# Optimization experiments

Measured on AMD Instinct MI355X. Metric: run time of the kernel, lower is better.

Reference implementation:

```python
import jax, jax.numpy as jnp
import numpy as np

DIM = 1024
HEADS = 16
HEAD_DIM = DIM // HEADS
LAYERS = 8
HIDDEN = 4 * DIM
VOCAB = 266
MAX_POS = 32768
B = 4
L = 2048
SCALE = HEAD_DIM ** -0.5
EPS = 1e-5


def layer_norm(x, g, b):
    m = jnp.mean(x, axis=-1, keepdims=True)
    v = jnp.mean(jnp.square(x - m), axis=-1, keepdims=True)
    return (x - m) * jax.lax.rsqrt(v + EPS) * g + b


def setup_inputs() -> dict:
    key = jax.random.key(0)
    ks = jax.random.split(key, 16)
    s = 0.02
    return {
        "tokens": jax.random.randint(ks[0], (B, L), 0, VOCAB),
        "tok_emb": jax.random.normal(ks[1], (VOCAB, DIM), jnp.float32) * s,
        "pos_emb": jax.random.normal(ks[2], (MAX_POS, DIM), jnp.float32) * s,
        "ln1_g": jnp.ones((LAYERS, DIM), jnp.float32),
        "ln1_b": jnp.zeros((LAYERS, DIM), jnp.float32),
        "q_w": jax.random.normal(ks[3], (LAYERS, DIM, DIM), jnp.float32) * s,
        "k_w": jax.random.normal(ks[4], (LAYERS, DIM, DIM), jnp.float32) * s,
        "v_w": jax.random.normal(ks[5], (LAYERS, DIM, DIM), jnp.float32) * s,
        "o_w": jax.random.normal(ks[6], (LAYERS, DIM, DIM), jnp.float32) * s,
        "ln2_g": jnp.ones((LAYERS, DIM), jnp.float32),
        "ln2_b": jnp.zeros((LAYERS, DIM), jnp.float32),
        "w1_w": jax.random.normal(ks[7], (LAYERS, HIDDEN, DIM), jnp.float32) * s,
        "wg_w": jax.random.normal(ks[8], (LAYERS, HIDDEN, DIM), jnp.float32) * s,
        "w2_w": jax.random.normal(ks[9], (LAYERS, DIM, HIDDEN), jnp.float32) * s,
        "lnf_g": jnp.ones((DIM,), jnp.float32),
        "lnf_b": jnp.zeros((DIM,), jnp.float32),
        "lm_w": jax.random.normal(ks[10], (VOCAB, DIM), jnp.float32) * s,
    }


def reference(tokens, tok_emb, pos_emb, ln1_g, ln1_b, q_w, k_w, v_w, o_w,
              ln2_g, ln2_b, w1_w, wg_w, w2_w, lnf_g, lnf_b, lm_w):
    Bv, Lv = tokens.shape
    x = tok_emb[tokens] + pos_emb[jnp.arange(Lv)][None, :, :]  # [B,L,D]
    # strictly-upper-triangular causal mask (True = masked)
    rows = jnp.arange(Lv)
    mask = rows[None, :] > rows[:, None]  # [L,L], col > row
    pos_bias = jnp.arange(Lv, dtype=x.dtype) * 0.01  # [L]
    neg_inf = jnp.array(-jnp.inf, dtype=x.dtype)

    for i in range(LAYERS):
        h = layer_norm(x, ln1_g[i], ln1_b[i])
        q = jnp.einsum('bld,ed->ble', h, q_w[i]).reshape(Bv, Lv, HEADS, HEAD_DIM).transpose(0, 2, 1, 3)
        k = jnp.einsum('bld,ed->ble', h, k_w[i]).reshape(Bv, Lv, HEADS, HEAD_DIM).transpose(0, 2, 1, 3)
        v = jnp.einsum('bld,ed->ble', h, v_w[i]).reshape(Bv, Lv, HEADS, HEAD_DIM).transpose(0, 2, 1, 3)
        attn = jnp.einsum('bhqd,bhkd->bhqk', q, k) * SCALE
        attn = jnp.where(mask[None, None, :, :], neg_inf, attn)
        attn = attn + pos_bias[None, None, None, :]
        attn = jax.nn.softmax(attn, axis=-1)
        out = jnp.einsum('bhqk,bhkd->bhqd', attn, v).transpose(0, 2, 1, 3).reshape(Bv, Lv, DIM)
        attn_out = jnp.einsum('bld,ed->ble', out, o_w[i])
        x = x + attn_out
        h2 = layer_norm(x, ln2_g[i], ln2_b[i])
        ff = jnp.einsum('blh,dh->bld', jax.nn.silu(jnp.einsum('bld,hd->blh', h2, w1_w[i])) * jnp.einsum('bld,hd->blh', h2, wg_w[i]), w2_w[i])
        x = x + ff

    last = layer_norm(x[:, -1, :], lnf_g, lnf_b)  # [B, D]
    return jnp.einsum('bd,vd->bv', last, lm_w)  # [B, VOCAB]
```

## Files before the change

### kernel.cpp

```cpp
#include <hip/hip_runtime.h>
#include <hip/hip_bf16.h>
#include <math.h>

#define DIMD 1024
#define HEADS 16
#define HD 64
#define LAYERS 8
#define HIDDEN 4096
#define VOCAB 266
#define NB 4
#define SEQ 2048
#define ROWS (NB*SEQ)
#define LOG2E 1.4426950408889634f
#define QSCALE (0.125f * LOG2E)
#define BIAS2 (0.01f * LOG2E)
#define THR2 8.0f

typedef float f32x4 __attribute__((ext_vector_type(4)));
typedef float f32x16 __attribute__((ext_vector_type(16)));
typedef __bf16 bf16x8 __attribute__((ext_vector_type(8)));
typedef __bf16 bf16x4 __attribute__((ext_vector_type(4)));

__device__ __forceinline__ f32x4 mfma16(bf16x8 a, bf16x8 b, f32x4 c) {
    return __builtin_amdgcn_mfma_f32_16x16x32_bf16(a, b, c, 0, 0, 0);
}
__device__ __forceinline__ f32x16 mfma32(bf16x8 a, bf16x8 b, f32x16 c) {
    return __builtin_amdgcn_mfma_f32_32x32x16_bf16(a, b, c, 0, 0, 0);
}

__device__ __forceinline__ void gload16(const __bf16* g, __bf16* l) {
    __builtin_amdgcn_global_load_lds(
        (const __attribute__((address_space(1))) void*)g,
        (__attribute__((address_space(3))) void*)l, 16, 0, 0);
}

__device__ __forceinline__ unsigned pack2(float a, float b) {
    union { __bf16 h[2]; unsigned u; } t;
    t.h[0] = (__bf16)a; t.h[1] = (__bf16)b;
    return t.u;
}
union PUN8 { unsigned u[4]; bf16x8 v; };

__global__ void embed_kernel(const int* __restrict__ tok, const float* __restrict__ te,
                             const float* __restrict__ pe, float* __restrict__ x) {
    int row = blockIdx.x;
    int t = tok[row];
    int l = row & (SEQ - 1);
    int c = threadIdx.x;
    f32x4 tv = *(const f32x4*)(te + (size_t)t * DIMD + c * 4);
    f32x4 pv = *(const f32x4*)(pe + (size_t)l * DIMD + c * 4);
    *(f32x4*)(x + (size_t)row * DIMD + c * 4) = tv + pv;
}

__global__ void cvt_kernel(const float* q, const float* k, const float* v, const float* o,
                           const float* w1, const float* wg, const float* w2,
                           __bf16* __restrict__ dst) {
    const size_t MM = 1024 * 1024;
    const float* src; size_t n; size_t off; int ilv = 0;
    switch (blockIdx.y) {
        case 0: src = q;  n = MM;     off = 0;       break;
        case 1: src = k;  n = MM;     off = MM;      break;
        case 2: src = v;  n = MM;     off = 2 * MM;  break;
        case 3: src = o;  n = MM;     off = 3 * MM;  break;
        case 4: src = w1; n = 4 * MM; off = 4 * MM;  ilv = 1; break;
        case 5: src = wg; n = 4 * MM; off = 4 * MM;  ilv = 2; break;
        default: src = w2; n = 4 * MM; off = 12 * MM; break;
    }
    size_t stride = (size_t)gridDim.x * blockDim.x * 8;
    for (size_t i = ((size_t)blockIdx.x * blockDim.x + threadIdx.x) * 8; i < n; i += stride) {
        f32x4 a = *(const f32x4*)(src + i);
        f32x4 b = *(const f32x4*)(src + i + 4);
        bf16x8 ov;
        ov[0] = (__bf16)a[0]; ov[1] = (__bf16)a[1]; ov[2] = (__bf16)a[2]; ov[3] = (__bf16)a[3];
        ov[4] = (__bf16)b[0]; ov[5] = (__bf16)b[1]; ov[6] = (__bf16)b[2]; ov[7] = (__bf16)b[3];
        size_t di;
        if (ilv) {
            size_t row = i >> 10, col = i & 1023;
            di = off + (((row << 1) | (ilv - 1)) << 10) + col;
        } else {
            di = off + i;
        }
        *(bf16x8*)(dst + di) = ov;
    }
}

template<bool F32OUT>
__global__ void ln_kernel(const float* __restrict__ xin, size_t row_stride,
                          const float* __restrict__ g, const float* __restrict__ bb,
                          void* __restrict__ out) {
    int row = blockIdx.x;
    int c = threadIdx.x;
    const float* xr = xin + (size_t)row * row_stride;
    f32x4 v = *(const f32x4*)(xr + c * 4);
    float s = v[0] + v[1] + v[2] + v[3];
    float s2 = v[0]*v[0] + v[1]*v[1] + v[2]*v[2] + v[3]*v[3];
    #pragma unroll
    for (int o = 32; o; o >>= 1) { s += __shfl_xor(s, o); s2 += __shfl_xor(s2, o); }
    __shared__ float red[8];
    int w = c >> 6, lane = c & 63;
    if (lane == 0) { red[w] = s; red[4 + w] = s2; }
    __syncthreads();
    s = red[0] + red[1] + red[2] + red[3];
    s2 = red[4] + red[5] + red[6] + red[7];
    float mean = s * (1.f / DIMD);
    float var = s2 * (1.f / DIMD) - mean * mean;
    float rstd = rsqrtf(var + 1e-5f);
    f32x4 gv = *(const f32x4*)(g + c * 4);
    f32x4 bv = *(const f32x4*)(bb + c * 4);
    f32x4 o4;
    #pragma unroll
    for (int j = 0; j < 4; ++j) o4[j] = (v[j] - mean) * rstd * gv[j] + bv[j];
    if (F32OUT) {
        *(f32x4*)((float*)out + (size_t)row * DIMD + c * 4) = o4;
    } else {
        bf16x4 hv;
        #pragma unroll
        for (int j = 0; j < 4; ++j) hv[j] = (__bf16)o4[j];
        *(bf16x4*)((__bf16*)out + (size_t)row * DIMD + c * 4) = hv;
    }
}

template<int EPI>
__global__ __launch_bounds__(256, 4)
void gemm_bt(const __bf16* __restrict__ A, const __bf16* __restrict__ W,
             int M, int N, int K,
             __bf16* bdst, float* fdst, float scale) {
    __shared__ __bf16 As[128 * 64];
    __shared__ __bf16 Bs[128 * 64];
    int tid = threadIdx.x;
    int lane = tid & 63, w = tid >> 6;
    int wm = w >> 1, wn = w & 1;
    int g16 = lane >> 4, l16 = lane & 15;
    int m0 = blockIdx.y * 128, n0 = blockIdx.x * 128;
    f32x4 acc[4][4] = {};
    int trow = tid >> 3;
    int cs8 = ((tid & 7) ^ (trow & 7)) * 8;
    const __bf16* ga = A + (size_t)(m0 + trow) * K + cs8;
    const __bf16* gb = W + (size_t)(n0 + trow) * K + cs8;
    int xsw = (l16 & 7) << 4;

    for (int k0 = 0; k0 < K; k0 += 64) {
        #pragma unroll
        for (int p = 0; p < 4; ++p) {
            gload16(ga + (size_t)(p * 32) * K + k0, As + (p * 256 + w * 64) * 8);
            gload16(gb + (size_t)(p * 32) * K + k0, Bs + (p * 256 + w * 64) * 8);
        }
        __syncthreads();
        #pragma unroll
        for (int kk = 0; kk < 2; ++kk) {
            bf16x8 af[4], bfv[4];
            #pragma unroll
            for (int f = 0; f < 4; ++f) {
                int ar = wm * 64 + f * 16 + l16;
                int br = wn * 64 + f * 16 + l16;
                af[f]  = *(const bf16x8*)((const char*)As + ((ar * 128 + kk * 64 + g16 * 16) ^ xsw));
                bfv[f] = *(const bf16x8*)((const char*)Bs + ((br * 128 + kk * 64 + g16 * 16) ^ xsw));
            }
            #pragma unroll
            for (int fm = 0; fm < 4; ++fm)
                #pragma unroll
                for (int fn = 0; fn < 4; ++fn)
                    acc[fm][fn] = mfma16(af[fm], bfv[fn], acc[fm][fn]);
        }
        __syncthreads();
    }

    #pragma unroll
    for (int fm = 0; fm < 4; ++fm) {
        int rbase = m0 + wm * 64 + fm * 16 + g16 * 4;
        #pragma unroll
        for (int fn = 0; fn < 4; ++fn) {
            int col = n0 + wn * 64 + fn * 16 + l16;
            if (EPI == 2) {
                #pragma unroll
                for (int j = 0; j < 4; ++j) {
                    size_t idx = (size_t)(rbase + j) * N + col;
                    fdst[idx] += acc[fm][fn][j];
                }
            } else if (EPI == 5) {
                int which = col >> 10;
                int c = col & 1023;
                int hh = c >> 6, d = c & 63;
                if (which == 2) {
                    int b = rbase >> 11, l = rbase & 2047;
                    __bf16* vp = bdst + 2 * (size_t)ROWS * DIMD;
                    bf16x4 hv;
                    #pragma unroll
                    for (int j = 0; j < 4; ++j) hv[j] = (__bf16)acc[fm][fn][j];
                    *(bf16x4*)(vp + ((size_t)(b * HEADS + hh) * HD + d) * SEQ + l) = hv;
                } else {
                    float sc = (which == 0) ? scale : 1.f;
                    __bf16* base = bdst + (size_t)which * ROWS * DIMD;
                    #pragma unroll
                    for (int j = 0; j < 4; ++j) {
                        int row = rbase + j;
                        int b = row >> 11, l = row & 2047;
                        base[(((size_t)(b * HEADS + hh) * SEQ + l) << 6) + d] =
                            (__bf16)(acc[fm][fn][j] * sc);
                    }
                }
            } else if (EPI == 6) {
                #pragma unroll
                for (int j = 0; j < 4; ++j) {
                    float own = acc[fm][fn][j];
                    float other = __shfl_xor(own, 1);
                    if (!(l16 & 1)) {
                        float si = own / (1.f + __expf(-own));
                        bdst[(size_t)(rbase + j) * (N >> 1) + (col >> 1)] = (__bf16)(si * other);
                    }
                }
            }
        }
    }
}

__global__ __launch_bounds__(256, 2)
void attn_kernel(const __bf16* __restrict__ qt, const __bf16* __restrict__ kt,
                 const __bf16* __restrict__ vt, __bf16* __restrict__ ao) {
    int qtile = 15 - (blockIdx.x >> 6);
    int g = blockIdx.x & 63;
    int hh = g & 15, b = g >> 4;
    int tid = threadIdx.x, lane = tid & 63, w = tid >> 6;
    int l32 = lane & 31, hi = lane >> 5;

    __shared__ __bf16 Ks[2][64 * 64];
    __shared__ __bf16 Vs[2][64 * 64];

    const __bf16* qbase = qt + (size_t)(b * HEADS + hh) * SEQ * HD;
    const __bf16* kbase = kt + (size_t)(b * HEADS + hh) * SEQ * HD;
    const __bf16* vbase = vt + (size_t)(b * HEADS + hh) * HD * SEQ;

    int rr = lane >> 3;
    int cs8 = ((lane & 7) ^ rr) * 8;

    int qb = qtile * 128;
    int nt = (qb >> 6) + 2;
    int qrow = qb + w * 32 + l32;
    int qrmax = qb + w * 32 + 31;

    bf16x8 qf[4];
    #pragma unroll
    for (int s = 0; s < 4; ++s)
        qf[s] = *(const bf16x8*)(qbase + (size_t)qrow * HD + s * 16 + hi * 8);

    f32x16 accO[2] = {};
    float m = -1e30f, lsum = 0.f;

    #pragma unroll
    for (int p = 0; p < 2; ++p) {
        int rbse = p * 32 + w * 8;
        gload16(kbase + (size_t)(rbse + rr) * HD + cs8, Ks[0] + rbse * 64);
        gload16(vbase + (size_t)(rbse + rr) * SEQ + cs8, Vs[0] + rbse * 64);
    }
    __syncthreads();

    for (int t = 0; t < nt; ++t) {
        int cur = t & 1;
        int kv0 = t << 6;

        if (t + 1 < nt) {
            int kv1 = kv0 + 64;
            #pragma unroll
            for (int p = 0; p < 2; ++p) {
                int rbse = p * 32 + w * 8;
                gload16(kbase + (size_t)(kv1 + rbse + rr) * HD + cs8, Ks[cur ^ 1] + rbse * 64);
                gload16(vbase + (size_t)(rbse + rr) * SEQ + kv1 + cs8, Vs[cur ^ 1] + rbse * 64);
            }
        }

        if (kv0 <= qrmax) {
            const char* Kb = (const char*)Ks[cur];
            const char* Vb = (const char*)Vs[cur];

            f32x16 sacc[2] = {};
            __builtin_amdgcn_s_setprio(1);
            #pragma unroll
            for (int kb = 0; kb < 2; ++kb) {
                int row = kb * 32 + l32;
                int rsw = row & 7;
                #pragma unroll
                for (int s = 0; s < 4; ++s) {
                    int cc = s * 2 + hi;
                    bf16x8 kf = *(const bf16x8*)(Kb + row * 128 + ((cc ^ rsw) << 4));
                    sacc[kb] = mfma32(kf, qf[s], sacc[kb]);
                }
            }
            __builtin_amdgcn_s_setprio(0);

            float mx = -1e30f;
            #pragma unroll
            for (int kb = 0; kb < 2; ++kb)
                #pragma unroll
                for (int r = 0; r < 16; ++r) {
                    int key = kv0 + kb * 32 + (r & 3) + 8 * (r >> 2) + 4 * hi;
                    float v = sacc[kb][r];
                    v = (key <= qrow) ? (v + BIAS2 * (float)key) : -1e30f;
                    sacc[kb][r] = v;
                    mx = fmaxf(mx, v);
                }
            mx = fmaxf(mx, __shfl_xor(mx, 32));

            if (!__all(mx <= m + THR2)) {
                float mnew = fmaxf(m, mx);
                float rs = exp2f(m - mnew);
                m = mnew; lsum *= rs;
                #pragma unroll
                for (int f = 0; f < 2; ++f)
                    #pragma unroll
                    for (int r = 0; r < 16; ++r) accO[f][r] *= rs;
            }

            #pragma unroll
            for (int kb = 0; kb < 2; ++kb) {
                float p[16];
                #pragma unroll
                for (int r = 0; r < 16; ++r) { p[r] = exp2f(sacc[kb][r] - m); lsum += p[r]; }
                #pragma unroll
                for (int s = 0; s < 2; ++s) {
                    unsigned a0 = pack2(p[s*8+0], p[s*8+1]);
                    unsigned a1 = pack2(p[s*8+2], p[s*8+3]);
                    unsigned b0 = pack2(p[s*8+4], p[s*8+5]);
                    unsigned b1 = pack2(p[s*8+6], p[s*8+7]);
                    unsigned xa0 = (unsigned)__shfl_xor((int)a0, 32);
                    unsigned xa1 = (unsigned)__shfl_xor((int)a1, 32);
                    unsigned xb0 = (unsigned)__shfl_xor((int)b0, 32);
                    unsigned xb1 = (unsigned)__shfl_xor((int)b1, 32);
                    PUN8 pf;
                    pf.u[0] = hi ? xb0 : a0;
                    pf.u[1] = hi ? xb1 : a1;
                    pf.u[2] = hi ? b0  : xa0;
                    pf.u[3] = hi ? b1  : xa1;
                    __builtin_amdgcn_s_setprio(1);
                    #pragma unroll
                    for (int f = 0; f < 2; ++f) {
                        int d = f * 32 + l32;
                        int cc = kb * 4 + s * 2 + hi;
                        bf16x8 vf = *(const bf16x8*)(Vb + d * 128 + ((cc ^ (d & 7)) << 4));
                        accO[f] = mfma32(vf, pf.v, accO[f]);
                    }
                    __builtin_amdgcn_s_setprio(0);
                }
            }
        }
        __syncthreads();
    }

    lsum += __shfl_xor(lsum, 32);
    float inv = 1.f / lsum;
    #pragma unroll
    for (int f = 0; f < 2; ++f)
        #pragma unroll
        for (int gI = 0; gI < 4; ++gI) {
            bf16x4 hv;
            #pragma unroll
            for (int j = 0; j < 4; ++j) hv[j] = (__bf16)(accO[f][gI * 4 + j] * inv);
            int d = f * 32 + 8 * gI + 4 * hi;
            *(bf16x4*)(ao + (size_t)(b * SEQ + qrow) * DIMD + hh * HD + d) = hv;
        }
}

__global__ void lm_head(const float* __restrict__ last, const float* __restrict__ lw,
                        float* __restrict__ out) {
    int v = blockIdx.x;
    int c = threadIdx.x, lane = c & 63, w = c >> 6;
    f32x4 wv = *(const f32x4*)(lw + (size_t)v * DIMD + c * 4);
    float a[NB];
    #pragma unroll
    for (int b = 0; b < NB; ++b) {
        f32x4 xv = *(const f32x4*)(last + b * DIMD + c * 4);
        a[b] = wv[0]*xv[0] + wv[1]*xv[1] + wv[2]*xv[2] + wv[3]*xv[3];
    }
    #pragma unroll
    for (int o = 32; o; o >>= 1)
        #pragma unroll
        for (int b = 0; b < NB; ++b) a[b] += __shfl_xor(a[b], o);
    __shared__ float red[4][NB];
    if (lane == 0)
        #pragma unroll
        for (int b = 0; b < NB; ++b) red[w][b] = a[b];
    __syncthreads();
    if (c < NB) {
        float s = red[0][c] + red[1][c] + red[2][c] + red[3][c];
        out[c * VOCAB + v] = s;
    }
}

extern "C" void kernel_launch(void* const* d_in, const int* in_sizes, int n_in,
                              void* d_out, int out_size, void* d_ws, size_t ws_size,
                              hipStream_t stream) {
    const int*   tokens  = (const int*)d_in[0];
    const float* tok_emb = (const float*)d_in[1];
    const float* pos_emb = (const float*)d_in[2];
    const float* ln1_g   = (const float*)d_in[3];
    const float* ln1_b   = (const float*)d_in[4];
    const float* q_w     = (const float*)d_in[5];
    const float* k_w     = (const float*)d_in[6];
    const float* v_w     = (const float*)d_in[7];
    const float* o_w     = (const float*)d_in[8];
    const float* ln2_g   = (const float*)d_in[9];
    const float* ln2_b   = (const float*)d_in[10];
    const float* w1_w    = (const float*)d_in[11];
    const float* wg_w    = (const float*)d_in[12];
    const float* w2_w    = (const float*)d_in[13];
    const float* lnf_g   = (const float*)d_in[14];
    const float* lnf_b   = (const float*)d_in[15];
    const float* lm_w    = (const float*)d_in[16];

    const size_t MM = 1024 * 1024;
    char* p = (char*)d_ws;
    __bf16* wbf = (__bf16*)p;          p += 16 * MM * 2;
    float*  x   = (float*)p;           p += (size_t)ROWS * DIMD * 4;
    __bf16* h   = (__bf16*)p;          p += (size_t)ROWS * DIMD * 2;
    __bf16* qt  = (__bf16*)p;          p += (size_t)ROWS * DIMD * 2;
    __bf16* kt  = (__bf16*)p;          p += (size_t)ROWS * DIMD * 2;
    __bf16* vt  = (__bf16*)p;          p += (size_t)ROWS * DIMD * 2;
    __bf16* ao  = (__bf16*)p;          p += (size_t)ROWS * DIMD * 2;
    __bf16* abuf= (__bf16*)p;          p += (size_t)ROWS * HIDDEN * 2;
    float*  last= (float*)p;           p += NB * DIMD * 4;

    embed_kernel<<<ROWS, 256, 0, stream>>>(tokens, tok_emb, pos_emb, x);

    for (int i = 0; i < LAYERS; ++i) {
        cvt_kernel<<<dim3(256, 7), 256, 0, stream>>>(
            q_w + (size_t)i * MM, k_w + (size_t)i * MM, v_w + (size_t)i * MM, o_w + (size_t)i * MM,
            w1_w + (size_t)i * 4 * MM, wg_w + (size_t)i * 4 * MM, w2_w + (size_t)i * 4 * MM, wbf);
        __bf16* wqkv = wbf;
        __bf16* wo   = wbf + 3 * MM;
        __bf16* w1g  = wbf + 4 * MM;
        __bf16* w2   = wbf + 12 * MM;

        ln_kernel<false><<<ROWS, 256, 0, stream>>>(x, DIMD, ln1_g + i * DIMD, ln1_b + i * DIMD, h);

        gemm_bt<5><<<dim3(24, 64), 256, 0, stream>>>(h, wqkv, ROWS, 3 * DIMD, DIMD, qt, nullptr, QSCALE);

        attn_kernel<<<1024, 256, 0, stream>>>(qt, kt, vt, ao);

        gemm_bt<2><<<dim3(8, 64), 256, 0, stream>>>(ao, wo, ROWS, DIMD, DIMD, nullptr, x, 1.f);

        ln_kernel<false><<<ROWS, 256, 0, stream>>>(x, DIMD, ln2_g + i * DIMD, ln2_b + i * DIMD, h);

        gemm_bt<6><<<dim3(64, 64), 256, 0, stream>>>(h, w1g, ROWS, 2 * HIDDEN, DIMD, abuf, nullptr, 1.f);

        gemm_bt<2><<<dim3(8, 64), 256, 0, stream>>>(abuf, w2, ROWS, DIMD, HIDDEN, nullptr, x, 1.f);
    }

    ln_kernel<true><<<NB, 256, 0, stream>>>(x + (size_t)(SEQ - 1) * DIMD, (size_t)SEQ * DIMD,
                                            lnf_g, lnf_b, last);
    lm_head<<<VOCAB, 256, 0, stream>>>(last, lm_w, (float*)d_out);
}
```

Before: 3.772 ms.

## Process two 32-row query chunks per wave to reuse K/V tiles in attention

Each attention block now covers a 256-row query band instead of 128, with every wave handling two 32-row query chunks that share each loaded K/V tile in LDS. The grid is halved to 512 blocks. This cuts K/V global loads and LDS staging per query row. In exchange it doubles accumulator and Q-fragment registers per wave, which may lower occupancy, and it gives fewer blocks with coarser causal load balance.

Result: slower. 4.005 ms (+6.2%).

```diff
diff --git a/kernel.cpp b/kernel.cpp
--- a/kernel.cpp
+++ b/kernel.cpp
@@ -217,7 +217,7 @@
 __global__ __launch_bounds__(256, 2)
 void attn_kernel(const __bf16* __restrict__ qt, const __bf16* __restrict__ kt,
                  const __bf16* __restrict__ vt, __bf16* __restrict__ ao) {
-    int qtile = 15 - (blockIdx.x >> 6);
+    int qband = 7 - (int)(blockIdx.x >> 6);
     int g = blockIdx.x & 63;
     int hh = g & 15, b = g >> 4;
     int tid = threadIdx.x, lane = tid & 63, w = tid >> 6;
@@ -233,18 +233,24 @@
     int rr = lane >> 3;
     int cs8 = ((lane & 7) ^ rr) * 8;
 
-    int qb = qtile * 128;
-    int nt = (qb >> 6) + 2;
-    int qrow = qb + w * 32 + l32;
-    int qrmax = qb + w * 32 + 31;
-
-    bf16x8 qf[4];
-    #pragma unroll
-    for (int s = 0; s < 4; ++s)
-        qf[s] = *(const bf16x8*)(qbase + (size_t)qrow * HD + s * 16 + hi * 8);
-
-    f32x16 accO[2] = {};
-    float m = -1e30f, lsum = 0.f;
+    int qb = qband * 256;
+    int nt = (qb >> 6) + 4;
+    int qrow[2], qrmax[2];
+    #pragma unroll
+    for (int c = 0; c < 2; ++c) {
+        qrow[c] = qb + (4 * c + w) * 32 + l32;
+        qrmax[c] = qb + (4 * c + w) * 32 + 31;
+    }
+
+    bf16x8 qf[2][4];
+    #pragma unroll
+    for (int c = 0; c < 2; ++c)
+        #pragma unroll
+        for (int s = 0; s < 4; ++s)
+            qf[c][s] = *(const bf16x8*)(qbase + (size_t)qrow[c] * HD + s * 16 + hi * 8);
+
+    f32x16 accO[2][2] = {};
+    float m[2] = {-1e30f, -1e30f}, lsum[2] = {0.f, 0.f};
 
     #pragma unroll
     for (int p = 0; p < 2; ++p) {
@@ -268,9 +274,12 @@
             }
         }
 
-        if (kv0 <= qrmax) {
-            const char* Kb = (const char*)Ks[cur];
-            const char* Vb = (const char*)Vs[cur];
+        const char* Kb = (const char*)Ks[cur];
+        const char* Vb = (const char*)Vs[cur];
+
+        #pragma unroll
+        for (int c = 0; c < 2; ++c) {
+            if (kv0 > qrmax[c]) continue;
 
             f32x16 sacc[2] = {};
             __builtin_amdgcn_s_setprio(1);
@@ -282,7 +291,7 @@
                 for (int s = 0; s < 4; ++s) {
                     int cc = s * 2 + hi;
                     bf16x8 kf = *(const bf16x8*)(Kb + row * 128 + ((cc ^ rsw) << 4));
-                    sacc[kb] = mfma32(kf, qf[s], sacc[kb]);
+                    sacc[kb] = mfma32(kf, qf[c][s], sacc[kb]);
                 }
             }
             __builtin_amdgcn_s_setprio(0);
@@ -294,27 +303,27 @@
                 for (int r = 0; r < 16; ++r) {
                     int key = kv0 + kb * 32 + (r & 3) + 8 * (r >> 2) + 4 * hi;
                     float v = sacc[kb][r];
-                    v = (key <= qrow) ? (v + BIAS2 * (float)key) : -1e30f;
+                    v = (key <= qrow[c]) ? (v + BIAS2 * (float)key) : -1e30f;
                     sacc[kb][r] = v;
                     mx = fmaxf(mx, v);
                 }
             mx = fmaxf(mx, __shfl_xor(mx, 32));
 
-            if (!__all(mx <= m + THR2)) {
-                float mnew = fmaxf(m, mx);
-                float rs = exp2f(m - mnew);
-                m = mnew; lsum *= rs;
+            if (!__all(mx <= m[c] + THR2)) {
+                float mnew = fmaxf(m[c], mx);
+                float rs = exp2f(m[c] - mnew);
+                m[c] = mnew; lsum[c] *= rs;
                 #pragma unroll
                 for (int f = 0; f < 2; ++f)
                     #pragma unroll
-                    for (int r = 0; r < 16; ++r) accO[f][r] *= rs;
+                    for (int r = 0; r < 16; ++r) accO[c][f][r] *= rs;
             }
 
             #pragma unroll
             for (int kb = 0; kb < 2; ++kb) {
                 float p[16];
                 #pragma unroll
-                for (int r = 0; r < 16; ++r) { p[r] = exp2f(sacc[kb][r] - m); lsum += p[r]; }
+                for (int r = 0; r < 16; ++r) { p[r] = exp2f(sacc[kb][r] - m[c]); lsum[c] += p[r]; }
                 #pragma unroll
                 for (int s = 0; s < 2; ++s) {
                     unsigned a0 = pack2(p[s*8+0], p[s*8+1]);
@@ -336,7 +345,7 @@
                         int d = f * 32 + l32;
                         int cc = kb * 4 + s * 2 + hi;
                         bf16x8 vf = *(const bf16x8*)(Vb + d * 128 + ((cc ^ (d & 7)) << 4));
-                        accO[f] = mfma32(vf, pf.v, accO[f]);
+                        accO[c][f] = mfma32(vf, pf.v, accO[c][f]);
                     }
                     __builtin_amdgcn_s_setprio(0);
                 }
@@ -345,18 +354,21 @@
         __syncthreads();
     }
 
-    lsum += __shfl_xor(lsum, 32);
-    float inv = 1.f / lsum;
-    #pragma unroll
-    for (int f = 0; f < 2; ++f)
-        #pragma unroll
-        for (int gI = 0; gI < 4; ++gI) {
-            bf16x4 hv;
-            #pragma unroll
-            for (int j = 0; j < 4; ++j) hv[j] = (__bf16)(accO[f][gI * 4 + j] * inv);
-            int d = f * 32 + 8 * gI + 4 * hi;
-            *(bf16x4*)(ao + (size_t)(b * SEQ + qrow) * DIMD + hh * HD + d) = hv;
-        }
+    #pragma unroll
+    for (int c = 0; c < 2; ++c) {
+        float l = lsum[c] + __shfl_xor(lsum[c], 32);
+        float inv = 1.f / l;
+        #pragma unroll
+        for (int f = 0; f < 2; ++f)
+            #pragma unroll
+            for (int gI = 0; gI < 4; ++gI) {
+                bf16x4 hv;
+                #pragma unroll
+                for (int j = 0; j < 4; ++j) hv[j] = (__bf16)(accO[c][f][gI * 4 + j] * inv);
+                int d = f * 32 + 8 * gI + 4 * hi;
+                *(bf16x4*)(ao + (size_t)(b * SEQ + qrow[c]) * DIMD + hh * HD + d) = hv;
+            }
+    }
 }
 
 __global__ void lm_head(const float* __restrict__ last, const float* __restrict__ lw,
@@ -433,7 +445,7 @@
 
         gemm_bt<5><<<dim3(24, 64), 256, 0, stream>>>(h, wqkv, ROWS, 3 * DIMD, DIMD, qt, nullptr, QSCALE);
 
-        attn_kernel<<<1024, 256, 0, stream>>>(qt, kt, vt, ao);
+        attn_kernel<<<512, 256, 0, stream>>>(qt, kt, vt, ao);
 
         gemm_bt<2><<<dim3(8, 64), 256, 0, stream>>>(ao, wo, ROWS, DIMD, DIMD, nullptr, x, 1.f);
 
```
